# Optimization experiments

Hardware: AMD Instinct MI355X
Metric: run time of the kernel (lower is better)

The kernel has to match this reference:

```python
import jax, jax.numpy as jnp
import numpy as np

RHO = 1.0          # ADMM penalty
LAM = 0.1          # lambda_sparse
MAX_ITERS = 20
ZETA = 0.05        # APAS drift threshold / CDS temperature
TAU = 0.1          # chiral stabilizer tolerance
STEP = 0.1         # gradient step size
COHESION = 1.0     # Mohr-Coulomb cohesion
MU = 0.5           # Mohr-Coulomb friction coefficient
DP_K = 10.0        # Drucker-Prager deviatoric-norm radius


def _pas(c):
    # Phase Alignment Invariant: scalar phase-coherence metric in [0,1]
    return jnp.abs(jnp.mean(jnp.cos(c)))


def _chirality(c):
    # odd (sign-sensitive) global moment
    return jnp.mean(c ** 3)


def _mc_proj(c, g):
    # Mohr-Coulomb yield projection: clamp magnitude to cohesion + mu*|grad|
    return jnp.sign(c) * jnp.minimum(jnp.abs(c), COHESION + MU * jnp.abs(g))


def _dp_proj(c):
    # Drucker-Prager: project deviatoric part onto norm ball of radius DP_K (per row)
    m = jnp.mean(c, axis=-1, keepdims=True)
    dev = c - m
    n = jnp.linalg.norm(dev, axis=-1, keepdims=True)
    scale = jnp.minimum(1.0, DP_K / (n + 1e-8))
    return m + dev * scale


def setup_inputs() -> dict:
    key = jax.random.key(0)
    k1, k2, k3 = jax.random.split(key, 3)
    B, D = 1024, 2048
    initial_c = 0.5 * jax.random.normal(k1, (B, D), dtype=jnp.float32)
    W = jax.random.normal(k2, (D, D), dtype=jnp.float32) / np.float32(np.sqrt(D))
    love_w = 1.0 + 0.01 * jax.random.normal(k3, (D,), dtype=jnp.float32)
    love_b = jnp.zeros((D,), dtype=jnp.float32)
    return {"initial_c": initial_c, "W": W, "love_w": love_w, "love_b": love_b}


def _forward(initial_c, W, love_w, love_b):
    c_sym = initial_c
    c0 = initial_c
    z0 = c0
    u0 = jnp.zeros_like(c0)
    prev_pas0 = _pas(c0)
    prev_score0 = -_chirality(c0)  # drift = 0 -> exp(0) = 1

    def step(carry, _):
        c, z, u, prev_pas, prev_score, low, done = carry

        def energy(ci):
            pred = ci @ W  # forward_op_fn
            violation_pressure = 0.5 * jnp.sum((pred - ci) ** 2)
            admm_tension = 0.5 * RHO * jnp.sum((ci - z + u) ** 2)
            return violation_pressure + admm_tension

        g = jax.grad(energy)(c)
        c_yield = _mc_proj(c, g)
        c_next = (c_yield * love_w + love_b) - STEP * g  # LoveVector then step
        z_in = c_next + u
        thr = LAM / RHO
        z_next = jnp.sign(z_in) * jnp.maximum(jnp.abs(z_in) - thr, 0.0)
        u_next = u + (c_next - z_next)

        cur_pas = _pas(c_next)
        drift = jnp.abs(cur_pas - prev_pas)
        violation = drift > ZETA
        low = jnp.where(cur_pas < 0.5, low + 1, 0)
        done = done | (low > 20)
        cur_score = -_chirality(c_next) * jnp.exp(-drift / ZETA)
        stable = (cur_score - prev_score) >= -TAU
        acc = (~violation) & stable & (~done)

        sel = lambda a, b: jnp.where(acc, a, b)
        new = (sel(c_next, c), sel(z_next, z), sel(u_next, u),
               jnp.where(acc, cur_pas, prev_pas),
               jnp.where(acc, cur_score, prev_score), low, done)
        return new, None

    init = (c0, z0, u0, prev_pas0, prev_score0,
            jnp.zeros((), jnp.int32), jnp.zeros((), jnp.bool_))
    (c_phys, z, u, _, _, _, _), _ = jax.lax.scan(step, init, None, length=MAX_ITERS)

    diff = jnp.linalg.norm(c_phys - c_sym)
    chi_cur = _chirality(c_phys)
    chi_orig = _chirality(c_sym)
    status = jnp.where(jnp.sign(chi_cur) != jnp.sign(chi_orig),
                       2,
                       jnp.where(diff > 5.0, 2, jnp.where(diff > 1.0, 1, 0))).astype(jnp.int32)

    delta = c_phys - c_sym
    symbolic_delta = jnp.round(delta * 10.0) / 10.0
    c_compressed = _dp_proj(c_sym + symbolic_delta)
    return c_compressed, status


def reference(initial_c, W, love_w, love_b):
    return _forward(initial_c, W, love_w, love_b)
```

## Files before the change

### kernel.cpp

```cpp
#include <hip/hip_runtime.h>
#include <math.h>

#define D 2048
#define BROWS 1024
#define NEL (D*BROWS)
#define NBLK 1024
#define NTHREADS_TOT (NBLK*256)

#define GM 64
#define GN 128
#define GK 16

__device__ __forceinline__ double blk_reduce(double v, double* sm) {
    const int t = threadIdx.x;
    sm[t] = v;
    __syncthreads();
    for (int s = 128; s > 0; s >>= 1) {
        if (t < s) sm[t] += sm[t + s];
        __syncthreads();
    }
    double r = sm[0];
    __syncthreads();
    return r;
}

__global__ __launch_bounds__(256, 2) void k_gemm(const float* __restrict__ A,
        const float* __restrict__ B, float* __restrict__ P0, float* __restrict__ P1,
        const float* __restrict__ Wadj, int ksz, int mode, const int* __restrict__ frz)
{
    if (frz && *frz) return;
    if (mode == 0 && (int)blockIdx.y < 2 * (int)blockIdx.x) return;
    __shared__ float As[2][GK][GM + 4];
    __shared__ float Bs[2][GK][GN + 4];
    const int t  = threadIdx.x;
    const int tx = t & 15, ty = t >> 4;
    const int row0 = blockIdx.y * GM, col0 = blockIdx.x * GN;
    const int k0 = blockIdx.z * ksz;
    float* __restrict__ out = blockIdx.z ? P1 : P0;

    const int wr = t >> 2, wq = t & 3;
    const float* pA  = A + (size_t)(row0 + wr) * D + (k0 + wq * 4);
    const float* pB0 = B + (size_t)(col0 + wr) * D + (k0 + wq * 4);
    const float* pB1 = B + (size_t)(col0 + 64 + wr) * D + (k0 + wq * 4);

    float acc[4][8];
    #pragma unroll
    for (int i = 0; i < 4; ++i)
        #pragma unroll
        for (int j = 0; j < 8; ++j) acc[i][j] = 0.0f;

    const int ntiles = ksz / GK;
    float4 ga, gb0, gb1;

#define LOADR { \
    ga  = *reinterpret_cast<const float4*>(pA);  \
    gb0 = *reinterpret_cast<const float4*>(pB0); \
    gb1 = *reinterpret_cast<const float4*>(pB1); \
    pA += GK; pB0 += GK; pB1 += GK; }

#define STAGE(BUF) { \
    As[BUF][wq*4+0][wr] = ga.x;  As[BUF][wq*4+1][wr] = ga.y;  \
    As[BUF][wq*4+2][wr] = ga.z;  As[BUF][wq*4+3][wr] = ga.w;  \
    Bs[BUF][wq*4+0][wr] = gb0.x; Bs[BUF][wq*4+1][wr] = gb0.y; \
    Bs[BUF][wq*4+2][wr] = gb0.z; Bs[BUF][wq*4+3][wr] = gb0.w; \
    Bs[BUF][wq*4+0][wr+64] = gb1.x; Bs[BUF][wq*4+1][wr+64] = gb1.y; \
    Bs[BUF][wq*4+2][wr+64] = gb1.z; Bs[BUF][wq*4+3][wr+64] = gb1.w; }

#define COMPUTE(BUF) { \
    _Pragma("unroll") \
    for (int k = 0; k < GK; ++k) { \
        float a[4], b[8]; \
        *reinterpret_cast<float4*>(&a[0]) = *reinterpret_cast<const float4*>(&As[BUF][k][ty*4]); \
        *reinterpret_cast<float4*>(&b[0]) = *reinterpret_cast<const float4*>(&Bs[BUF][k][tx*4]); \
        *reinterpret_cast<float4*>(&b[4]) = *reinterpret_cast<const float4*>(&Bs[BUF][k][64 + tx*4]); \
        _Pragma("unroll") \
        for (int i = 0; i < 4; ++i) \
            _Pragma("unroll") \
            for (int j = 0; j < 8; ++j) \
                acc[i][j] += a[i] * b[j]; \
    } }

    LOADR;
    STAGE(0);
    __syncthreads();

    for (int tt = 0; tt < ntiles; tt += 2) {
        LOADR;
        COMPUTE(0);
        STAGE(1);
        __syncthreads();
        if (tt + 2 < ntiles) {
            LOADR;
            COMPUTE(1);
            STAGE(0);
            __syncthreads();
        } else {
            COMPUTE(1);
        }
    }

#undef LOADR
#undef STAGE
#undef COMPUTE

    #pragma unroll
    for (int i = 0; i < 4; ++i) {
        const int grow = row0 + ty*4 + i;
        float vv[8];
        #pragma unroll
        for (int j = 0; j < 8; ++j) vv[j] = acc[i][j];
        if (mode == 0) {
            #pragma unroll
            for (int j = 0; j < 8; ++j) {
                const int gcol = col0 + ((j < 4) ? (tx*4 + j) : (64 + tx*4 + j - 4));
                const float wsum = Wadj[(size_t)grow * D + gcol] + Wadj[(size_t)gcol * D + grow];
                vv[j] += (grow == gcol ? 1.0f : 0.0f) - wsum;
            }
        }
        float* orow = &out[(size_t)grow * D + col0];
        *reinterpret_cast<float4*>(&orow[tx*4]) =
            make_float4(vv[0], vv[1], vv[2], vv[3]);
        *reinterpret_cast<float4*>(&orow[64 + tx*4]) =
            make_float4(vv[4], vv[5], vv[6], vv[7]);
    }
}

__global__ __launch_bounds__(256) void k_mirror(float* __restrict__ M)
{
    const int C = blockIdx.x, R = blockIdx.y;
    if (R < C) return;
    __shared__ float T[64][68];
    const int t = threadIdx.x;
    const int r = t >> 4, c4 = t & 15;
    #pragma unroll
    for (int p = 0; p < 4; ++p) {
        const int rr = r + p * 16;
        const float4 v = *reinterpret_cast<const float4*>(&M[(size_t)(R*64 + rr) * D + C*64 + c4*4]);
        T[c4*4+0][rr] = v.x; T[c4*4+1][rr] = v.y;
        T[c4*4+2][rr] = v.z; T[c4*4+3][rr] = v.w;
    }
    __syncthreads();
    if (R == C) {
        #pragma unroll
        for (int p = 0; p < 4; ++p) {
            const int rr = r + p * 16;
            #pragma unroll
            for (int q = 0; q < 4; ++q) {
                const int cc = c4*4 + q;
                if (rr < cc) M[(size_t)(R*64 + rr) * D + C*64 + cc] = T[rr][cc];
            }
        }
    } else {
        #pragma unroll
        for (int p = 0; p < 4; ++p) {
            const int rr = r + p * 16;
            *reinterpret_cast<float4*>(&M[(size_t)(C*64 + rr) * D + R*64 + c4*4]) =
                make_float4(T[rr][c4*4+0], T[rr][c4*4+1], T[rr][c4*4+2], T[rr][c4*4+3]);
        }
    }
}

__global__ __launch_bounds__(256) void k_init(const float* __restrict__ c0,
        float* __restrict__ c, float* __restrict__ z, float* __restrict__ u,
        double* __restrict__ partials)
{
    __shared__ double sm[256];
    double sc = 0.0, s3 = 0.0;
    const int tid = blockIdx.x * 256 + threadIdx.x;
    const float4 zero4 = make_float4(0.f, 0.f, 0.f, 0.f);
    for (int i4 = tid; i4 < NEL/4; i4 += NTHREADS_TOT) {
        const float4 v4 = reinterpret_cast<const float4*>(c0)[i4];
        reinterpret_cast<float4*>(c)[i4] = v4;
        reinterpret_cast<float4*>(z)[i4] = v4;
        reinterpret_cast<float4*>(u)[i4] = zero4;
        const float va[4] = {v4.x, v4.y, v4.z, v4.w};
        #pragma unroll
        for (int L = 0; L < 4; ++L) {
            sc += (double)cosf(va[L]);
            s3 += (double)((va[L] * va[L]) * va[L]);
        }
    }
    const double tc = blk_reduce(sc, sm);
    const double t3 = blk_reduce(s3, sm);
    if (threadIdx.x == 0) { partials[blockIdx.x] = tc; partials[NBLK + blockIdx.x] = t3; }
}

__global__ __launch_bounds__(256) void k_decide0(const double* __restrict__ partials,
        double* __restrict__ scal, int* __restrict__ flag, int* __restrict__ frz,
        int* __restrict__ sel)
{
    __shared__ double sm[256];
    const int t = threadIdx.x;
    const double a = partials[t] + partials[t+256] + partials[t+512] + partials[t+768];
    const double b = partials[NBLK+t] + partials[NBLK+t+256] + partials[NBLK+t+512] + partials[NBLK+t+768];
    const double tc = blk_reduce(a, sm);
    const double t3 = blk_reduce(b, sm);
    if (t == 0) {
        const double pas = fabs(tc / (double)NEL);
        const double chi = t3 / (double)NEL;
        scal[0] = pas; scal[1] = -chi; scal[2] = chi;
        *flag = 0; *frz = 0; *sel = 0;
    }
}

__global__ __launch_bounds__(256) void k_elem_pp(const float* __restrict__ P0,
        const float* __restrict__ P1, const float* __restrict__ cc,
        float* __restrict__ cn, float* __restrict__ z, float* __restrict__ u,
        const float* __restrict__ lw, const float* __restrict__ lb,
        double* __restrict__ partials, const int* __restrict__ frz)
{
#pragma clang fp contract(off)
    if (*frz) return;
    __shared__ double sm[256];
    double sc = 0.0, s3 = 0.0;
    const int tid = blockIdx.x * 256 + threadIdx.x;
    for (int i4 = tid; i4 < NEL/4; i4 += NTHREADS_TOT) {
        const int j4 = i4 & (D/4 - 1);
        const float4 p0 = reinterpret_cast<const float4*>(P0)[i4];
        const float4 p1 = reinterpret_cast<const float4*>(P1)[i4];
        const float4 cv4 = reinterpret_cast<const float4*>(cc)[i4];
        const float4 zv4 = reinterpret_cast<const float4*>(z)[i4];
        const float4 uv4 = reinterpret_cast<const float4*>(u)[i4];
        const float4 w4 = reinterpret_cast<const float4*>(lw)[j4];
        const float4 b4 = reinterpret_cast<const float4*>(lb)[j4];
        const float p0a[4] = {p0.x, p0.y, p0.z, p0.w};
        const float p1a[4] = {p1.x, p1.y, p1.z, p1.w};
        const float cva[4] = {cv4.x, cv4.y, cv4.z, cv4.w};
        const float zva[4] = {zv4.x, zv4.y, zv4.z, zv4.w};
        const float uva[4] = {uv4.x, uv4.y, uv4.z, uv4.w};
        const float w4a[4] = {w4.x, w4.y, w4.z, w4.w};
        const float b4a[4] = {b4.x, b4.y, b4.z, b4.w};
        float Rc[4], Rz[4], Ru[4];
        #pragma unroll
        for (int L = 0; L < 4; ++L) {
            const float cv = cva[L];
            const float uv = uva[L];
            const float g = (p0a[L] + p1a[L]) + ((cv - zva[L]) + uv);
            const float lim = 1.0f + 0.5f * fabsf(g);
            const float mn = fminf(fabsf(cv), lim);
            const float cy = (cv > 0.0f) ? mn : ((cv < 0.0f) ? -mn : 0.0f);
            const float cnv = (cy * w4a[L] + b4a[L]) - 0.1f * g;
            Rc[L] = cnv;
            const float zi = cnv + uv;
            float zm = fabsf(zi) - 0.1f;
            zm = fmaxf(zm, 0.0f);
            const float zn = (zi > 0.0f) ? zm : ((zi < 0.0f) ? -zm : 0.0f);
            Rz[L] = zn;
            Ru[L] = uv + (cnv - zn);
            sc += (double)cosf(cnv);
            s3 += (double)((cnv * cnv) * cnv);
        }
        reinterpret_cast<float4*>(cn)[i4] = make_float4(Rc[0], Rc[1], Rc[2], Rc[3]);
        reinterpret_cast<float4*>(z)[i4]  = make_float4(Rz[0], Rz[1], Rz[2], Rz[3]);
        reinterpret_cast<float4*>(u)[i4]  = make_float4(Ru[0], Ru[1], Ru[2], Ru[3]);
    }
    const double tc = blk_reduce(sc, sm);
    const double t3 = blk_reduce(s3, sm);
    if (threadIdx.x == 0) { partials[blockIdx.x] = tc; partials[NBLK + blockIdx.x] = t3; }
}

__global__ __launch_bounds__(256) void k_elem(float* __restrict__ P0,
        const float* __restrict__ P1, const float* __restrict__ c,
        const float* __restrict__ z, const float* __restrict__ u,
        const float* __restrict__ lw, const float* __restrict__ lb,
        double* __restrict__ partials, const int* __restrict__ frz)
{
#pragma clang fp contract(off)
    if (*frz) return;
    __shared__ double sm[256];
    double sc = 0.0, s3 = 0.0;
    const int tid = blockIdx.x * 256 + threadIdx.x;
    for (int i = tid; i < NEL; i += NTHREADS_TOT) {
        const int j = i & (D - 1);
        const float cv = c[i];
        const float g = (P0[i] + P1[i]) + ((cv - z[i]) + u[i]);
        const float lim = 1.0f + 0.5f * fabsf(g);
        const float mn = fminf(fabsf(cv), lim);
        const float cy = (cv > 0.0f) ? mn : ((cv < 0.0f) ? -mn : 0.0f);
        const float cnv = (cy * lw[j] + lb[j]) - 0.1f * g;
        P0[i] = cnv;
        sc += (double)cosf(cnv);
        s3 += (double)((cnv * cnv) * cnv);
    }
    const double tc = blk_reduce(sc, sm);
    const double t3 = blk_reduce(s3, sm);
    if (threadIdx.x == 0) { partials[blockIdx.x] = tc; partials[NBLK + blockIdx.x] = t3; }
}

__global__ __launch_bounds__(256) void k_decide(const double* __restrict__ partials,
        double* __restrict__ scal, int* __restrict__ flag, int* __restrict__ frz,
        int* __restrict__ sel, int next_sel)
{
    __shared__ double sm[256];
    if (*frz) return;
    const int t = threadIdx.x;
    const double a = partials[t] + partials[t+256] + partials[t+512] + partials[t+768];
    const double b = partials[NBLK+t] + partials[NBLK+t+256] + partials[NBLK+t+512] + partials[NBLK+t+768];
    const double tc = blk_reduce(a, sm);
    const double t3 = blk_reduce(b, sm);
    if (t == 0) {
        const double pas = fabs(tc / (double)NEL);
        const double drift = fabs(pas - scal[0]);
        const double chi = t3 / (double)NEL;
        const double score = -chi * exp(-drift / 0.05);
        const bool violation = drift > 0.05;
        const bool stable = (score - scal[1]) >= -0.1;
        const int acc = (!violation && stable) ? 1 : 0;
        *flag = acc;
        if (acc) { scal[0] = pas; scal[1] = score; *sel = next_sel; }
        else     { *frz = 1; }
    }
}

__global__ __launch_bounds__(256) void k_commit(const float* __restrict__ cn,
        float* __restrict__ c, float* __restrict__ z, float* __restrict__ u,
        const int* __restrict__ flag)
{
#pragma clang fp contract(off)
    if (*flag == 0) return;
    const int tid = blockIdx.x * 256 + threadIdx.x;
    for (int i = tid; i < NEL; i += NTHREADS_TOT) {
        const float cnv = cn[i];
        const float uv = u[i];
        const float zi = cnv + uv;
        float zm = fabsf(zi) - 0.1f;
        zm = fmaxf(zm, 0.0f);
        const float zn = (zi > 0.0f) ? zm : ((zi < 0.0f) ? -zm : 0.0f);
        c[i] = cnv;
        z[i] = zn;
        u[i] = uv + (cnv - zn);
    }
}

__global__ __launch_bounds__(256) void k_final_rows(const float* __restrict__ c0,
        const float* __restrict__ cA, const float* __restrict__ cB,
        const int* __restrict__ sel, float* __restrict__ outp)
{
#pragma clang fp contract(off)
    __shared__ double sm[256];
    const float* __restrict__ c = (*sel) ? cB : cA;
    const int row = blockIdx.x;
    const size_t base = (size_t)row * D;
    float tv[8];
    double s1 = 0.0;
    #pragma unroll
    for (int s = 0; s < 8; ++s) {
        const int j = threadIdx.x + s * 256;
        const float s0 = c0[base + j];
        const float delta = c[base + j] - s0;
        const float sym = rintf(delta * 10.0f) / 10.0f;
        const float tval = s0 + sym;
        tv[s] = tval;
        s1 += (double)tval;
    }
    const double tot = blk_reduce(s1, sm);
    const float m = (float)(tot / (double)D);
    double s2 = 0.0;
    #pragma unroll
    for (int s = 0; s < 8; ++s) {
        const float dev = tv[s] - m;
        s2 += (double)(dev * dev);
    }
    const double tot2 = blk_reduce(s2, sm);
    const float n = sqrtf((float)tot2);
    const float scale = fminf(1.0f, 10.0f / (n + 1e-8f));
    #pragma unroll
    for (int s = 0; s < 8; ++s) {
        const int j = threadIdx.x + s * 256;
        outp[base + j] = m + (tv[s] - m) * scale;
    }
}

__global__ __launch_bounds__(256) void k_final_glob(const float* __restrict__ c0,
        const float* __restrict__ cA, const float* __restrict__ cB,
        const int* __restrict__ sel, double* __restrict__ partials)
{
    __shared__ double sm[256];
    const float* __restrict__ c = (*sel) ? cB : cA;
    double s3 = 0.0, sd = 0.0;
    const int tid = blockIdx.x * 256 + threadIdx.x;
    for (int i = tid; i < NEL; i += NTHREADS_TOT) {
        const float v = c[i];
        s3 += (double)((v * v) * v);
        const float d = v - c0[i];
        sd += (double)(d * d);
    }
    const double t3 = blk_reduce(s3, sm);
    const double td = blk_reduce(sd, sm);
    if (threadIdx.x == 0) { partials[blockIdx.x] = t3; partials[NBLK + blockIdx.x] = td; }
}

__global__ __launch_bounds__(256) void k_final_status(const double* __restrict__ partials,
        const double* __restrict__ scal, float* __restrict__ outp)
{
    __shared__ double sm[256];
    const int t = threadIdx.x;
    const double a = partials[t] + partials[t+256] + partials[t+512] + partials[t+768];
    const double b = partials[NBLK+t] + partials[NBLK+t+256] + partials[NBLK+t+512] + partials[NBLK+t+768];
    const double t3 = blk_reduce(a, sm);
    const double td = blk_reduce(b, sm);
    if (t == 0) {
        const double chi_cur = t3 / (double)NEL;
        const double diff = sqrt(td);
        const double chi_orig = scal[2];
        const int s_cur = (chi_cur > 0.0) - (chi_cur < 0.0);
        const int s_org = (chi_orig > 0.0) - (chi_orig < 0.0);
        int status;
        if (s_cur != s_org)   status = 2;
        else if (diff > 5.0)  status = 2;
        else if (diff > 1.0)  status = 1;
        else                  status = 0;
        outp[NEL] = (float)status;
    }
}

extern "C" void kernel_launch(void* const* d_in, const int* in_sizes, int n_in,
                              void* d_out, int out_size, void* d_ws, size_t ws_size,
                              hipStream_t stream)
{
    const float* c0 = (const float*)d_in[0];
    const float* W  = (const float*)d_in[1];
    const float* lw = (const float*)d_in[2];
    const float* lb = (const float*)d_in[3];
    float* outp = (float*)d_out;

    const size_t M4 = (size_t)D * D;
    const size_t N4 = (size_t)NEL;
    float* Mb = (float*)d_ws;
    float* region = Mb + M4;

    const size_t tail_bytes = (2 * NBLK + 8) * sizeof(double) + 4 * sizeof(int);
    const bool pp = ws_size >= (M4 + 6 * N4) * sizeof(float) + tail_bytes;

    float *cA, *cB, *z, *u, *P0, *P1;
    if (pp) { cA = region; cB = cA + N4; z = cB + N4; u = z + N4; P0 = u + N4; P1 = P0 + N4; }
    else    { cA = region; cB = cA;      z = cA + N4; u = z + N4; P0 = u + N4; P1 = P0 + N4; }
    double* partials = (double*)(P1 + N4);
    double* scal = partials + 2 * NBLK;
    int* flag = (int*)(scal + 8);
    int* frz  = flag + 1;
    int* sel  = frz + 1;

    k_gemm<<<dim3(D / GN, D / GM, 1), 256, 0, stream>>>(W, W, Mb, Mb, W, D, 0, nullptr);
    k_mirror<<<dim3(D / 64, D / 64), 256, 0, stream>>>(Mb);
    k_init<<<NBLK, 256, 0, stream>>>(c0, cA, z, u, partials);
    k_decide0<<<1, 256, 0, stream>>>(partials, scal, flag, frz, sel);

    for (int t = 0; t < 20; ++t) {
        const float* ccur = (pp && (t & 1)) ? cB : cA;
        float* cnxt = (pp && !(t & 1)) ? cB : cA;
        k_gemm<<<dim3(D / GN, BROWS / GM, 2), 256, 0, stream>>>(ccur, Mb, P0, P1, nullptr, D / 2, 1, frz);
        if (pp) {
            k_elem_pp<<<NBLK, 256, 0, stream>>>(P0, P1, ccur, cnxt, z, u, lw, lb, partials, frz);
            k_decide<<<1, 256, 0, stream>>>(partials, scal, flag, frz, sel, (t + 1) & 1);
        } else {
            k_elem<<<NBLK, 256, 0, stream>>>(P0, P1, cA, z, u, lw, lb, partials, frz);
            k_decide<<<1, 256, 0, stream>>>(partials, scal, flag, frz, sel, 0);
            k_commit<<<NBLK, 256, 0, stream>>>(P0, cA, z, u, flag);
        }
    }

    k_final_rows<<<BROWS, 256, 0, stream>>>(c0, cA, cB, sel, outp);
    k_final_glob<<<NBLK, 256, 0, stream>>>(c0, cA, cB, sel, partials);
    k_final_status<<<1, 256, 0, stream>>>(partials, scal, outp);
}
```

Measured before the change: 2.864 ms.

## Fuse ADMM iteration loop into one persistent cooperative kernel with grid syncs

```diff
diff --git a/kernel.cpp b/kernel.cpp
--- a/kernel.cpp
+++ b/kernel.cpp
@@ -1,11 +1,16 @@
 #include <hip/hip_runtime.h>
+#include <hip/hip_cooperative_groups.h>
 #include <math.h>
+
+namespace cg = cooperative_groups;
 
 #define D 2048
 #define BROWS 1024
 #define NEL (D*BROWS)
 #define NBLK 1024
 #define NTHREADS_TOT (NBLK*256)
+#define CBLK 512
+#define CTHREADS (CBLK*256)
 
 #define GM 64
 #define GN 128
@@ -23,34 +28,6 @@
     __syncthreads();
     return r;
 }
-
-__global__ __launch_bounds__(256, 2) void k_gemm(const float* __restrict__ A,
-        const float* __restrict__ B, float* __restrict__ P0, float* __restrict__ P1,
-        const float* __restrict__ Wadj, int ksz, int mode, const int* __restrict__ frz)
-{
-    if (frz && *frz) return;
-    if (mode == 0 && (int)blockIdx.y < 2 * (int)blockIdx.x) return;
-    __shared__ float As[2][GK][GM + 4];
-    __shared__ float Bs[2][GK][GN + 4];
-    const int t  = threadIdx.x;
-    const int tx = t & 15, ty = t >> 4;
-    const int row0 = blockIdx.y * GM, col0 = blockIdx.x * GN;
-    const int k0 = blockIdx.z * ksz;
-    float* __restrict__ out = blockIdx.z ? P1 : P0;
-
-    const int wr = t >> 2, wq = t & 3;
-    const float* pA  = A + (size_t)(row0 + wr) * D + (k0 + wq * 4);
-    const float* pB0 = B + (size_t)(col0 + wr) * D + (k0 + wq * 4);
-    const float* pB1 = B + (size_t)(col0 + 64 + wr) * D + (k0 + wq * 4);
-
-    float acc[4][8];
-    #pragma unroll
-    for (int i = 0; i < 4; ++i)
-        #pragma unroll
-        for (int j = 0; j < 8; ++j) acc[i][j] = 0.0f;
-
-    const int ntiles = ksz / GK;
-    float4 ga, gb0, gb1;
 
 #define LOADR { \
     ga  = *reinterpret_cast<const float4*>(pA);  \
@@ -80,28 +57,40 @@
                 acc[i][j] += a[i] * b[j]; \
     } }
 
-    LOADR;
-    STAGE(0);
-    __syncthreads();
-
+__global__ __launch_bounds__(256, 2) void k_gemm(const float* __restrict__ A,
+        const float* __restrict__ B, float* __restrict__ P0, float* __restrict__ P1,
+        const float* __restrict__ Wadj, int ksz, int mode, const int* __restrict__ frz)
+{
+    if (frz && *frz) return;
+    if (mode == 0 && (int)blockIdx.y < 2 * (int)blockIdx.x) return;
+    __shared__ float As[2][GK][GM + 4];
+    __shared__ float Bs[2][GK][GN + 4];
+    const int t  = threadIdx.x;
+    const int tx = t & 15, ty = t >> 4;
+    const int row0 = blockIdx.y * GM, col0 = blockIdx.x * GN;
+    const int k0 = blockIdx.z * ksz;
+    float* __restrict__ out = blockIdx.z ? P1 : P0;
+
+    const int wr = t >> 2, wq = t & 3;
+    const float* pA  = A + (size_t)(row0 + wr) * D + (k0 + wq * 4);
+    const float* pB0 = B + (size_t)(col0 + wr) * D + (k0 + wq * 4);
+    const float* pB1 = B + (size_t)(col0 + 64 + wr) * D + (k0 + wq * 4);
+
+    float acc[4][8];
+    #pragma unroll
+    for (int i = 0; i < 4; ++i)
+        #pragma unroll
+        for (int j = 0; j < 8; ++j) acc[i][j] = 0.0f;
+
+    const int ntiles = ksz / GK;
+    float4 ga, gb0, gb1;
+
+    LOADR; STAGE(0); __syncthreads();
     for (int tt = 0; tt < ntiles; tt += 2) {
-        LOADR;
-        COMPUTE(0);
-        STAGE(1);
-        __syncthreads();
-        if (tt + 2 < ntiles) {
-            LOADR;
-            COMPUTE(1);
-            STAGE(0);
-            __syncthreads();
-        } else {
-            COMPUTE(1);
-        }
-    }
-
-#undef LOADR
-#undef STAGE
-#undef COMPUTE
+        LOADR; COMPUTE(0); STAGE(1); __syncthreads();
+        if (tt + 2 < ntiles) { LOADR; COMPUTE(1); STAGE(0); __syncthreads(); }
+        else                 { COMPUTE(1); }
+    }
 
     #pragma unroll
     for (int i = 0; i < 4; ++i) {
@@ -124,6 +113,139 @@
             make_float4(vv[4], vv[5], vv[6], vv[7]);
     }
 }
+
+__global__ __launch_bounds__(256, 2) void k_iter(float* __restrict__ P0,
+        float* __restrict__ P1, float* __restrict__ cA, float* __restrict__ cB,
+        float* __restrict__ z, float* __restrict__ u,
+        const float* __restrict__ lw, const float* __restrict__ lb,
+        double* __restrict__ partials, const double* __restrict__ scal,
+        int* __restrict__ sel, const float* __restrict__ Mb)
+{
+    __shared__ float As[2][GK][GM + 4];
+    __shared__ float Bs[2][GK][GN + 4];
+    __shared__ double sm[256];
+    cg::grid_group grid = cg::this_grid();
+
+    const int t  = threadIdx.x;
+    const int tx = t & 15, ty = t >> 4;
+    const int bid = blockIdx.x;
+    const int bx = bid & 15, by = (bid >> 4) & 15, bz = bid >> 8;
+    const int row0 = by * GM, col0 = bx * GN;
+    const int k0 = bz * (D / 2);
+    float* __restrict__ out = bz ? P1 : P0;
+    const int wr = t >> 2, wq = t & 3;
+    const int gtid = bid * 256 + t;
+
+    double prev_pas = scal[0];
+    double prev_score = scal[1];
+
+    for (int it = 0; it < 20; ++it) {
+        const float* __restrict__ ccur = (it & 1) ? cB : cA;
+        float* __restrict__ cnxt = (it & 1) ? cA : cB;
+
+        {
+            const float* pA  = ccur + (size_t)(row0 + wr) * D + (k0 + wq * 4);
+            const float* pB0 = Mb + (size_t)(col0 + wr) * D + (k0 + wq * 4);
+            const float* pB1 = Mb + (size_t)(col0 + 64 + wr) * D + (k0 + wq * 4);
+            float acc[4][8];
+            #pragma unroll
+            for (int i = 0; i < 4; ++i)
+                #pragma unroll
+                for (int j = 0; j < 8; ++j) acc[i][j] = 0.0f;
+            const int ntiles = (D / 2) / GK;
+            float4 ga, gb0, gb1;
+            LOADR; STAGE(0); __syncthreads();
+            for (int tt = 0; tt < ntiles; tt += 2) {
+                LOADR; COMPUTE(0); STAGE(1); __syncthreads();
+                if (tt + 2 < ntiles) { LOADR; COMPUTE(1); STAGE(0); __syncthreads(); }
+                else                 { COMPUTE(1); }
+            }
+            #pragma unroll
+            for (int i = 0; i < 4; ++i) {
+                const int grow = row0 + ty*4 + i;
+                float* orow = &out[(size_t)grow * D + col0];
+                *reinterpret_cast<float4*>(&orow[tx*4]) =
+                    make_float4(acc[i][0], acc[i][1], acc[i][2], acc[i][3]);
+                *reinterpret_cast<float4*>(&orow[64 + tx*4]) =
+                    make_float4(acc[i][4], acc[i][5], acc[i][6], acc[i][7]);
+            }
+            __syncthreads();
+        }
+        grid.sync();
+
+        {
+#pragma clang fp contract(off)
+            double sc = 0.0, s3 = 0.0;
+            for (int i4 = gtid; i4 < NEL/4; i4 += CTHREADS) {
+                const int j4 = i4 & (D/4 - 1);
+                const float4 p0 = reinterpret_cast<const float4*>(P0)[i4];
+                const float4 p1 = reinterpret_cast<const float4*>(P1)[i4];
+                const float4 cv4 = reinterpret_cast<const float4*>(ccur)[i4];
+                const float4 zv4 = reinterpret_cast<const float4*>(z)[i4];
+                const float4 uv4 = reinterpret_cast<const float4*>(u)[i4];
+                const float4 w4 = reinterpret_cast<const float4*>(lw)[j4];
+                const float4 b4 = reinterpret_cast<const float4*>(lb)[j4];
+                const float p0a[4] = {p0.x, p0.y, p0.z, p0.w};
+                const float p1a[4] = {p1.x, p1.y, p1.z, p1.w};
+                const float cva[4] = {cv4.x, cv4.y, cv4.z, cv4.w};
+                const float zva[4] = {zv4.x, zv4.y, zv4.z, zv4.w};
+                const float uva[4] = {uv4.x, uv4.y, uv4.z, uv4.w};
+                const float w4a[4] = {w4.x, w4.y, w4.z, w4.w};
+                const float b4a[4] = {b4.x, b4.y, b4.z, b4.w};
+                float Rc[4], Rz[4], Ru[4];
+                #pragma unroll
+                for (int L = 0; L < 4; ++L) {
+                    const float cv = cva[L];
+                    const float uv = uva[L];
+                    const float g = (p0a[L] + p1a[L]) + ((cv - zva[L]) + uv);
+                    const float lim = 1.0f + 0.5f * fabsf(g);
+                    const float mn = fminf(fabsf(cv), lim);
+                    const float cy = (cv > 0.0f) ? mn : ((cv < 0.0f) ? -mn : 0.0f);
+                    const float cnv = (cy * w4a[L] + b4a[L]) - 0.1f * g;
+                    Rc[L] = cnv;
+                    const float zi = cnv + uv;
+                    float zm = fabsf(zi) - 0.1f;
+                    zm = fmaxf(zm, 0.0f);
+                    const float zn = (zi > 0.0f) ? zm : ((zi < 0.0f) ? -zm : 0.0f);
+                    Rz[L] = zn;
+                    Ru[L] = uv + (cnv - zn);
+                    sc += (double)cosf(cnv);
+                    s3 += (double)((cnv * cnv) * cnv);
+                }
+                reinterpret_cast<float4*>(cnxt)[i4] = make_float4(Rc[0], Rc[1], Rc[2], Rc[3]);
+                reinterpret_cast<float4*>(z)[i4]  = make_float4(Rz[0], Rz[1], Rz[2], Rz[3]);
+                reinterpret_cast<float4*>(u)[i4]  = make_float4(Ru[0], Ru[1], Ru[2], Ru[3]);
+            }
+            const double tc = blk_reduce(sc, sm);
+            const double t3 = blk_reduce(s3, sm);
+            if (t == 0) { partials[bid] = tc; partials[NBLK + bid] = t3; }
+        }
+        grid.sync();
+
+        {
+            const double a = partials[t] + partials[t + 256];
+            const double b = partials[NBLK + t] + partials[NBLK + t + 256];
+            const double tc = blk_reduce(a, sm);
+            const double t3 = blk_reduce(b, sm);
+            const double pas = fabs(tc / (double)NEL);
+            const double drift = fabs(pas - prev_pas);
+            const double chi = t3 / (double)NEL;
+            const double score = -chi * exp(-drift / 0.05);
+            const bool violation = drift > 0.05;
+            const bool stable = (score - prev_score) >= -0.1;
+            if (!violation && stable) {
+                prev_pas = pas; prev_score = score;
+                if (bid == 0 && t == 0) *sel = (it + 1) & 1;
+            } else {
+                break;
+            }
+        }
+    }
+}
+
+#undef LOADR
+#undef STAGE
+#undef COMPUTE
 
 __global__ __launch_bounds__(256) void k_mirror(float* __restrict__ M)
 {
@@ -259,34 +381,6 @@
     if (threadIdx.x == 0) { partials[blockIdx.x] = tc; partials[NBLK + blockIdx.x] = t3; }
 }
 
-__global__ __launch_bounds__(256) void k_elem(float* __restrict__ P0,
-        const float* __restrict__ P1, const float* __restrict__ c,
-        const float* __restrict__ z, const float* __restrict__ u,
-        const float* __restrict__ lw, const float* __restrict__ lb,
-        double* __restrict__ partials, const int* __restrict__ frz)
-{
-#pragma clang fp contract(off)
-    if (*frz) return;
-    __shared__ double sm[256];
-    double sc = 0.0, s3 = 0.0;
-    const int tid = blockIdx.x * 256 + threadIdx.x;
-    for (int i = tid; i < NEL; i += NTHREADS_TOT) {
-        const int j = i & (D - 1);
-        const float cv = c[i];
-        const float g = (P0[i] + P1[i]) + ((cv - z[i]) + u[i]);
-        const float lim = 1.0f + 0.5f * fabsf(g);
-        const float mn = fminf(fabsf(cv), lim);
-        const float cy = (cv > 0.0f) ? mn : ((cv < 0.0f) ? -mn : 0.0f);
-        const float cnv = (cy * lw[j] + lb[j]) - 0.1f * g;
-        P0[i] = cnv;
-        sc += (double)cosf(cnv);
-        s3 += (double)((cnv * cnv) * cnv);
-    }
-    const double tc = blk_reduce(sc, sm);
-    const double t3 = blk_reduce(s3, sm);
-    if (threadIdx.x == 0) { partials[blockIdx.x] = tc; partials[NBLK + blockIdx.x] = t3; }
-}
-
 __global__ __launch_bounds__(256) void k_decide(const double* __restrict__ partials,
         double* __restrict__ scal, int* __restrict__ flag, int* __restrict__ frz,
         int* __restrict__ sel, int next_sel)
@@ -312,26 +406,6 @@
     }
 }
 
-__global__ __launch_bounds__(256) void k_commit(const float* __restrict__ cn,
-        float* __restrict__ c, float* __restrict__ z, float* __restrict__ u,
-        const int* __restrict__ flag)
-{
-#pragma clang fp contract(off)
-    if (*flag == 0) return;
-    const int tid = blockIdx.x * 256 + threadIdx.x;
-    for (int i = tid; i < NEL; i += NTHREADS_TOT) {
-        const float cnv = cn[i];
-        const float uv = u[i];
-        const float zi = cnv + uv;
-        float zm = fabsf(zi) - 0.1f;
-        zm = fmaxf(zm, 0.0f);
-        const float zn = (zi > 0.0f) ? zm : ((zi < 0.0f) ? -zm : 0.0f);
-        c[i] = cnv;
-        z[i] = zn;
-        u[i] = uv + (cnv - zn);
-    }
-}
-
 __global__ __launch_bounds__(256) void k_final_rows(const float* __restrict__ c0,
         const float* __restrict__ cA, const float* __restrict__ cB,
         const int* __restrict__ sel, float* __restrict__ outp)
@@ -446,17 +520,23 @@
     k_init<<<NBLK, 256, 0, stream>>>(c0, cA, z, u, partials);
     k_decide0<<<1, 256, 0, stream>>>(partials, scal, flag, frz, sel);
 
-    for (int t = 0; t < 20; ++t) {
-        const float* ccur = (pp && (t & 1)) ? cB : cA;
-        float* cnxt = (pp && !(t & 1)) ? cB : cA;
-        k_gemm<<<dim3(D / GN, BROWS / GM, 2), 256, 0, stream>>>(ccur, Mb, P0, P1, nullptr, D / 2, 1, frz);
-        if (pp) {
+    bool done = false;
+    if (pp) {
+        void* args[] = { &P0, &P1, &cA, &cB, &z, &u,
+                         (void*)&lw, (void*)&lb, &partials, &scal, &sel, &Mb };
+        hipError_t err = hipLaunchCooperativeKernel(
+            reinterpret_cast<void*>(k_iter), dim3(CBLK), dim3(256), args, 0, stream);
+        if (err == hipSuccess) done = true;
+        else (void)hipGetLastError();
+    }
+
+    if (!done) {
+        for (int t = 0; t < 20; ++t) {
+            const float* ccur = (pp && (t & 1)) ? cB : cA;
+            float* cnxt = (pp && !(t & 1)) ? cB : cA;
+            k_gemm<<<dim3(D / GN, BROWS / GM, 2), 256, 0, stream>>>(ccur, Mb, P0, P1, nullptr, D / 2, 1, frz);
             k_elem_pp<<<NBLK, 256, 0, stream>>>(P0, P1, ccur, cnxt, z, u, lw, lb, partials, frz);
             k_decide<<<1, 256, 0, stream>>>(partials, scal, flag, frz, sel, (t + 1) & 1);
-        } else {
-            k_elem<<<NBLK, 256, 0, stream>>>(P0, P1, cA, z, u, lw, lb, partials, frz);
-            k_decide<<<1, 256, 0, stream>>>(partials, scal, flag, frz, sel, 0);
-            k_commit<<<NBLK, 256, 0, stream>>>(P0, cA, z, u, flag);
         }
     }
 
```

Measured after the change: 5.099 ms. 1.78x slower.
